# Optimization experiments

Measured on AMD Instinct MI355X. Metric: run time of the kernel, lower is better.

The kernel has to match this reference:

```python
import jax, jax.numpy as jnp
import numpy as np

N = 20000      # nodes
E = 50000      # edges
B = 128        # graphs in batch
H = 64         # hidden_dim
FEAT = 28      # raw node feature dim
N_TYPES = 100  # one-hot size for node_type
EDGE_DIM = 5   # one-hot size for edge_type
OUT = 1        # output_dim
MP_ITER = 3
S2S_ITER = 4


def setup_inputs() -> dict:
    key = jax.random.key(0)
    ks = jax.random.split(key, 24)
    s = 0.05
    inp = {
        'node_feat': jax.random.normal(ks[0], (N, FEAT), dtype=jnp.float32),
        'node_type': jax.random.randint(ks[1], (N,), 0, N_TYPES),
        'edge_index': jax.random.randint(ks[2], (2, E), 0, N),
        'edge_type': jax.random.randint(ks[3], (E,), 0, EDGE_DIM),
        'batch': jnp.sort(jax.random.randint(ks[4], (N,), 0, B)),
        # node embedding
        'W_emb': jax.random.normal(ks[5], (N_TYPES + FEAT, H), dtype=jnp.float32) * s,
        'b_emb': jnp.zeros((H,), dtype=jnp.float32),
        # shared edge net: edge_dim -> H -> H*H
        'W_e1': jax.random.normal(ks[6], (EDGE_DIM, H), dtype=jnp.float32) * s,
        'b_e1': jnp.zeros((H,), dtype=jnp.float32),
        'W_e2': jax.random.normal(ks[7], (H, H * H), dtype=jnp.float32) * s,
        'b_e2': jnp.zeros((H * H,), dtype=jnp.float32),
        # per-layer NNConv root weight + bias
        'roots': jax.random.normal(ks[8], (MP_ITER, H, H), dtype=jnp.float32) * s,
        'conv_bias': jnp.zeros((MP_ITER, H), dtype=jnp.float32),
        # Set2Set LSTM (input 2H, hidden H); torch gate order i,f,g,o
        'W_ih': jax.random.normal(ks[9], (4 * H, 2 * H), dtype=jnp.float32) * s,
        'W_hh': jax.random.normal(ks[10], (4 * H, H), dtype=jnp.float32) * s,
        'b_ih': jnp.zeros((4 * H,), dtype=jnp.float32),
        'b_hh': jnp.zeros((4 * H,), dtype=jnp.float32),
        # output MLP 2H -> H -> OUT
        'W_o1': jax.random.normal(ks[11], (2 * H, H), dtype=jnp.float32) * s,
        'b_o1': jnp.zeros((H,), dtype=jnp.float32),
        'W_o2': jax.random.normal(ks[12], (H, OUT), dtype=jnp.float32) * s,
        'b_o2': jnp.zeros((OUT,), dtype=jnp.float32),
    }
    return inp


def _forward(node_feat, W_emb, b_emb, W_e1, b_e1, W_e2, b_e2, roots, conv_bias,
             W_ih, W_hh, b_ih, b_hh, W_o1, b_o1, W_o2, b_o2,
             node_type, edge_index, edge_type, batch):
    # node embedding: [one_hot(node_type,100) ; node_feat] @ W_emb
    x_in = jnp.concatenate(
        [jax.nn.one_hot(node_type, N_TYPES, dtype=node_feat.dtype), node_feat], axis=-1)
    h = x_in @ W_emb + b_emb                                   # [N, H]

    # edge-conditioned weights (edge_attr is fixed, edge_net is shared across
    # iterations, so nn(edge_attr) is identical each layer -> compute once)
    edge_attr = jax.nn.one_hot(edge_type, EDGE_DIM, dtype=node_feat.dtype)
    Wmat = jax.nn.relu(edge_attr @ W_e1 + b_e1) @ W_e2 + b_e2  # [E, H*H]
    Wmat = Wmat.reshape(E, H, H)                               # [E, H_in, H_out]

    src, dst = edge_index[0], edge_index[1]
    for i in range(MP_ITER):
        msg = jnp.einsum('eh,eho->eo', h[src], Wmat)           # per-edge matvec
        agg = jax.ops.segment_sum(msg, dst, num_segments=N)    # sum aggregation
        h = agg + h @ roots[i] + conv_bias[i]                  # NNConv root + bias

    # Set2Set pooling
    hx = jnp.zeros((B, H), dtype=h.dtype)
    cx = jnp.zeros((B, H), dtype=h.dtype)
    q_star = jnp.zeros((B, 2 * H), dtype=h.dtype)
    for _ in range(S2S_ITER):
        gates = q_star @ W_ih.T + b_ih + hx @ W_hh.T + b_hh
        ig, fg, gg, og = jnp.split(gates, 4, axis=-1)
        cx = jax.nn.sigmoid(fg) * cx + jax.nn.sigmoid(ig) * jnp.tanh(gg)
        hx = jax.nn.sigmoid(og) * jnp.tanh(cx)
        q = hx                                                 # [B, H]
        e = jnp.sum(h * q[batch], axis=-1)                     # [N]
        m = jax.lax.stop_gradient(jax.ops.segment_max(e, batch, num_segments=B))
        a = jnp.exp(e - m[batch])
        denom = jax.ops.segment_sum(a, batch, num_segments=B)
        denom = jnp.where(denom == 0, 1.0, denom)
        a = a / denom[batch]                                   # scatter softmax
        r = jax.ops.segment_sum(a[:, None] * h, batch, num_segments=B)  # [B, H]
        q_star = jnp.concatenate([q, r], axis=-1)

    out = jax.nn.relu(q_star @ W_o1 + b_o1) @ W_o2 + b_o2      # [B, OUT]
    return out


def reference(node_feat, node_type, edge_index, edge_type, batch,
              W_emb, b_emb, W_e1, b_e1, W_e2, b_e2, roots, conv_bias,
              W_ih, W_hh, b_ih, b_hh, W_o1, b_o1, W_o2, b_o2):
    return _forward(node_feat, W_emb, b_emb, W_e1, b_e1, W_e2, b_e2, roots,
                    conv_bias, W_ih, W_hh, b_ih, b_hh, W_o1, b_o1, W_o2, b_o2,
                    node_type, edge_index, edge_type, batch)
```

## Files before the change

### kernel.cpp

```cpp
#include <hip/hip_runtime.h>
#include <math.h>


#define NN 20000
#define NE 50000
#define NB 128
#define HD 64
#define NFEAT 28
#define NTYPES 100
#define EDIM 5
#define MPIT 3
#define S2SIT 4
#define NBLK_E ((NE + 255) / 256)
#define SMAX 224
#define HP (HD + 1)
#define EPW 7

__device__ __forceinline__ float sigm(float x) {
  return 1.0f / (1.0f + expf(-x));
}

__device__ __forceinline__ float rdlane(float v, int l) {
  return __uint_as_float(__builtin_amdgcn_readlane(__float_as_uint(v), l));
}

__global__ __launch_bounds__(256) void k_pre(
    const int* __restrict__ batch, const int* __restrict__ etype,
    int* __restrict__ gstart, int* __restrict__ bc) {
  __shared__ int wcc[4][EDIM];
  const int tid = threadIdx.x;
  const int lane = tid & 63;
  const int wv = tid >> 6;
  const int blk = blockIdx.x;
  const int gtid = (blk << 8) + tid;
  const int nthr = gridDim.x << 8;

  if (blk < NBLK_E) {
    int e = (blk << 8) + tid;
    int ty = (e < NE) ? etype[e] : -1;
    #pragma unroll
    for (int t = 0; t < EDIM; ++t) {
      unsigned long long m = __ballot(ty == t);
      if (lane == 0) wcc[wv][t] = __popcll(m);
    }
    __syncthreads();
    if (tid < EDIM)
      bc[blk * EDIM + tid] = wcc[0][tid] + wcc[1][tid] + wcc[2][tid] + wcc[3][tid];
  }

  for (int n = gtid; n < NN; n += nthr) {
    int b = batch[n];
    if (n == 0)
      for (int t = 0; t <= b; ++t) gstart[t] = 0;
    int bn = (n + 1 < NN) ? batch[n + 1] : NB;
    for (int t = b + 1; t <= bn; ++t) gstart[t] = n + 1;
  }
}

__global__ __launch_bounds__(256) void k_main(
    const float* __restrict__ feat, const int* __restrict__ ntype,
    const int* __restrict__ etype, const int* __restrict__ ei,
    const float* __restrict__ W_emb, const float* __restrict__ b_emb,
    const float* __restrict__ W_e1, const float* __restrict__ b_e1,
    const float* __restrict__ W_e2, const float* __restrict__ b_e2,
    const float* __restrict__ W_ih, const float* __restrict__ W_hh,
    const int* __restrict__ bc,
    float* __restrict__ Wty, float* __restrict__ hA, float* __restrict__ hB,
    float* __restrict__ W_ihT, float* __restrict__ W_hhT,
    int2* __restrict__ sd) {
  __shared__ float sv[EDIM][HD];
  __shared__ float red[4][EDIM][HD];
  __shared__ int s_base[EDIM];
  __shared__ int wc[4][EDIM];
  const int tid = threadIdx.x;
  const int lane = tid & 63;
  const int wv = tid >> 6;
  const int blk = blockIdx.x;
  const int nblk = gridDim.x;
  const int nthr = nblk << 8;
  const int gtid = (blk << 8) + tid;
  const int gw = (blk << 2) + wv;
  const int nwave = nblk << 2;

  if (blk < 64) {
    int mbase = blk * 64;
    for (int idx = tid; idx < EDIM * HD; idx += 256) {
      int t = idx >> 6, j = idx & 63;
      float x = W_e1[t * HD + j] + b_e1[j];
      sv[t][j] = x > 0.f ? x : 0.f;
    }
    __syncthreads();
    int l = tid & 63, jg = tid >> 6;
    float acc[EDIM] = {0.f, 0.f, 0.f, 0.f, 0.f};
    #pragma unroll
    for (int jj = 0; jj < 16; ++jj) {
      int j = jg * 16 + jj;
      float w2 = W_e2[j * 4096 + mbase + l];
      #pragma unroll
      for (int t = 0; t < EDIM; ++t) acc[t] = fmaf(sv[t][j], w2, acc[t]);
    }
    #pragma unroll
    for (int t = 0; t < EDIM; ++t) red[jg][t][l] = acc[t];
    __syncthreads();
    for (int idx = tid; idx < EDIM * HD; idx += 256) {
      int t = idx >> 6, m = idx & 63;
      float s = red[0][t][m] + red[1][t][m] + red[2][t][m] + red[3][t][m];
      Wty[t * 4096 + mbase + m] = s + b_e2[mbase + m];
    }
  }

  if (blk >= 64 && blk < 64 + NBLK_E) {
    int pblk = blk - 64;
    if (wv == 0) {
      int part[EDIM], tot[EDIM];
      #pragma unroll
      for (int t = 0; t < EDIM; ++t) { part[t] = 0; tot[t] = 0; }
      for (int b = lane; b < NBLK_E; b += 64) {
        #pragma unroll
        for (int t = 0; t < EDIM; ++t) {
          int x = bc[b * EDIM + t];
          tot[t] += x;
          if (b < pblk) part[t] += x;
        }
      }
      #pragma unroll
      for (int t = 0; t < EDIM; ++t) {
        #pragma unroll
        for (int off = 32; off; off >>= 1) {
          tot[t]  += __shfl_xor(tot[t],  off, 64);
          part[t] += __shfl_xor(part[t], off, 64);
        }
      }
      if (lane == 0) {
        int run = 0;
        #pragma unroll
        for (int t = 0; t < EDIM; ++t) {
          s_base[t] = run + part[t];
          run += tot[t];
        }
      }
    }
    int e = (pblk << 8) + tid;
    int ty = (e < NE) ? etype[e] : -1;
    int svv = 0, dv = 0;
    if (e < NE) { svv = ei[e]; dv = ei[NE + e]; }
    int rank = 0;
    #pragma unroll
    for (int t = 0; t < EDIM; ++t) {
      unsigned long long m = __ballot(ty == t);
      if (lane == 0) wc[wv][t] = __popcll(m);
      if (ty == t) rank = __popcll(m & ((1ull << lane) - 1ull));
    }
    __syncthreads();
    if (ty >= 0) {
      int base = s_base[ty];
      for (int w = 0; w < wv; ++w) base += wc[w][ty];
      sd[base + rank] = make_int2(svv | (ty << 16), dv);
    }
  }

  for (int o = gtid; o < 2 * HD * 4 * HD; o += nthr)
    W_ihT[o] = W_ih[(o & 255) * 128 + (o >> 8)];
  for (int o = gtid; o < HD * 4 * HD; o += nthr)
    W_hhT[o] = W_hh[(o & 255) * 64 + (o >> 8)];

  {
    float wf[NFEAT];
    #pragma unroll
    for (int f = 0; f < NFEAT; ++f) wf[f] = W_emb[(NTYPES + f) * HD + lane];
    float bb = b_emb[lane];
    for (int n = gw; n < NN; n += nwave) {
      int nu = __builtin_amdgcn_readfirstlane(n);
      int t = __builtin_amdgcn_readfirstlane(ntype[nu]);
      const float* row = feat + nu * NFEAT;
      float acc = bb + W_emb[t * HD + lane];
      #pragma unroll
      for (int f = 0; f < NFEAT; ++f) acc = fmaf(row[f], wf[f], acc);
      hA[nu * HD + lane] = acc;
    }
  }

  {
    float4 z = make_float4(0.f, 0.f, 0.f, 0.f);
    for (int i = gtid; i < NN * HD / 4; i += nthr)
      reinterpret_cast<float4*>(hB)[i] = z;
  }
}

__global__ __launch_bounds__(256) void k_mp(
    const int2* __restrict__ sd,
    const float* __restrict__ Wty, const float* __restrict__ hsrc,
    float* __restrict__ htgt, float* __restrict__ hzero,
    const float* __restrict__ root, const float* __restrict__ bias) {
  const int lane = threadIdx.x & 63;
  const int wv = threadIdx.x >> 6;
  const int blk = blockIdx.x;

  if (blk < 512) {
    float w[HD];
    #pragma unroll
    for (int k = 0; k < HD; ++k) w[k] = root[k * HD + lane];
    float bb = bias[lane];
    int rw = (blk << 2) + wv;
    for (int n = rw; n < NN; n += 2048) {
      int nu = __builtin_amdgcn_readfirstlane(n);
      const float* row = hsrc + nu * HD;
      float a0 = bb, a1 = 0.f, a2 = 0.f, a3 = 0.f;
      #pragma unroll
      for (int k = 0; k < HD; k += 4) {
        a0 = fmaf(row[k + 0], w[k + 0], a0);
        a1 = fmaf(row[k + 1], w[k + 1], a1);
        a2 = fmaf(row[k + 2], w[k + 2], a2);
        a3 = fmaf(row[k + 3], w[k + 3], a3);
      }
      atomicAdd(&htgt[nu * HD + lane], (a0 + a1) + (a2 + a3));
    }
    if (hzero) {
      float4 z = make_float4(0.f, 0.f, 0.f, 0.f);
      for (int i = (blk << 8) + threadIdx.x; i < NN * HD / 4; i += 512 * 256)
        reinterpret_cast<float4*>(hzero)[i] = z;
    }
  } else {
    int wid = ((blk - 512) << 2) + wv;
    int beg = wid * EPW;
    if (beg >= NE) return;
    int len = NE - beg; if (len > EPW) len = EPW;

    int2 ed = sd[beg + (lane < len ? lane : len - 1)];

    float hv[EPW];
    #pragma unroll
    for (int j = 0; j < EPW; ++j) {
      int sx = __builtin_amdgcn_readlane(ed.x, j < EPW ? j : 0);
      hv[j] = hsrc[(sx & 0xFFFF) * HD + lane];
    }

    int curt = -1;
    float w[HD];
    #pragma unroll
    for (int j = 0; j < EPW; ++j) {
      if (j >= len) break;
      int ex = __builtin_amdgcn_readlane(ed.x, j);
      int dj = __builtin_amdgcn_readlane(ed.y, j);
      int ty = ex >> 16;
      if (ty != curt) {
        curt = ty;
        #pragma unroll
        for (int k = 0; k < HD; ++k) w[k] = Wty[ty * 4096 + k * HD + lane];
      }
      float a0 = 0.f, a1 = 0.f, a2 = 0.f, a3 = 0.f;
      #pragma unroll
      for (int k = 0; k < HD; k += 4) {
        a0 = fmaf(rdlane(hv[j], k + 0), w[k + 0], a0);
        a1 = fmaf(rdlane(hv[j], k + 1), w[k + 1], a1);
        a2 = fmaf(rdlane(hv[j], k + 2), w[k + 2], a2);
        a3 = fmaf(rdlane(hv[j], k + 3), w[k + 3], a3);
      }
      atomicAdd(&htgt[dj * HD + lane], (a0 + a1) + (a2 + a3));
    }
  }
}

__global__ __launch_bounds__(256) void k_s2s(
    const float* __restrict__ h, const int* __restrict__ gstart,
    const float* __restrict__ W_ihT, const float* __restrict__ W_hhT,
    const float* __restrict__ b_ih, const float* __restrict__ b_hh,
    const float* __restrict__ W_o1, const float* __restrict__ b_o1,
    const float* __restrict__ W_o2, const float* __restrict__ b_o2,
    float* __restrict__ out) {
  __shared__ float hs[SMAX * HP];
  __shared__ float ebuf[SMAX];
  __shared__ float qstar[2 * HD];
  __shared__ float hxs[HD], cxs[HD], gates[4 * HD];
  __shared__ float redM[4], redS[4], redR[4][HD];
  __shared__ float hid[HD];
  int b = blockIdx.x;
  int tid = threadIdx.x;
  int lane = tid & 63, wv = tid >> 6;

  int st = gstart[b], en = gstart[b + 1];
  int cnt = en - st;
  int cached = cnt < SMAX ? cnt : SMAX;

  int total = cached * HD;
  for (int base = tid * 4; base < total; base += 1024) {
    float4 v = *reinterpret_cast<const float4*>(h + st * HD + base);
    int n = base >> 6, k = base & 63;
    float* row = hs + n * HP + k;
    row[0] = v.x; row[1] = v.y; row[2] = v.z; row[3] = v.w;
  }
  if (tid < 2 * HD) qstar[tid] = 0.f;
  if (tid < HD) { hxs[tid] = 0.f; cxs[tid] = 0.f; }
  __syncthreads();

  for (int it = 0; it < S2SIT; ++it) {
    float acc0 = b_ih[tid] + b_hh[tid], acc1 = 0.f;
    #pragma unroll 8
    for (int j = 0; j < 2 * HD; j += 2) {
      acc0 = fmaf(qstar[j],     W_ihT[j * 256 + tid],       acc0);
      acc1 = fmaf(qstar[j + 1], W_ihT[(j + 1) * 256 + tid], acc1);
    }
    #pragma unroll 8
    for (int j = 0; j < HD; j += 2) {
      acc0 = fmaf(hxs[j],     W_hhT[j * 256 + tid],       acc0);
      acc1 = fmaf(hxs[j + 1], W_hhT[(j + 1) * 256 + tid], acc1);
    }
    gates[tid] = acc0 + acc1;
    __syncthreads();
    if (tid < HD) {
      float ig = sigm(gates[tid]);
      float fg = sigm(gates[HD + tid]);
      float gg = tanhf(gates[2 * HD + tid]);
      float og = sigm(gates[3 * HD + tid]);
      float c = fmaf(fg, cxs[tid], ig * gg);
      cxs[tid] = c;
      hxs[tid] = og * tanhf(c);
    }
    __syncthreads();

    float e = -1e30f;
    if (tid < cached) {
      const float* row = hs + tid * HP;
      float d0 = 0.f, d1 = 0.f;
      #pragma unroll 8
      for (int k = 0; k < HD; k += 2) {
        d0 = fmaf(row[k],     hxs[k],     d0);
        d1 = fmaf(row[k + 1], hxs[k + 1], d1);
      }
      e = d0 + d1;
      ebuf[tid] = e;
    }
    float m = e;
    #pragma unroll
    for (int off = 32; off; off >>= 1) m = fmaxf(m, __shfl_xor(m, off, 64));
    float qreg = hxs[lane];
    for (int n = cached + wv; n < cnt; n += 4) {
      float ev = h[(st + n) * HD + lane] * qreg;
      #pragma unroll
      for (int off = 32; off; off >>= 1) ev += __shfl_xor(ev, off, 64);
      m = fmaxf(m, ev);
    }
    if (lane == 0) redM[wv] = m;
    __syncthreads();
    float M = fmaxf(fmaxf(redM[0], redM[1]), fmaxf(redM[2], redM[3]));

    float sp = 0.f;
    if (tid < cached) {
      float a = expf(ebuf[tid] - M);
      ebuf[tid] = a;
      sp = a;
    }
    #pragma unroll
    for (int off = 32; off; off >>= 1) sp += __shfl_xor(sp, off, 64);
    __syncthreads();

    float r = 0.f;
    for (int n = wv; n < cached; n += 4)
      r = fmaf(ebuf[n], hs[n * HP + lane], r);
    float s_tail = 0.f;
    for (int n = cached + wv; n < cnt; n += 4) {
      float v = h[(st + n) * HD + lane];
      float ev = v * qreg;
      #pragma unroll
      for (int off = 32; off; off >>= 1) ev += __shfl_xor(ev, off, 64);
      float a = expf(ev - M);
      s_tail += a;
      r = fmaf(a, v, r);
    }
    if (lane == 0) redS[wv] = sp + s_tail;
    redR[wv][lane] = r;
    __syncthreads();
    if (tid < HD) {
      float S = redS[0] + redS[1] + redS[2] + redS[3];
      float R = redR[0][tid] + redR[1][tid] + redR[2][tid] + redR[3][tid];
      if (S == 0.f) S = 1.f;
      qstar[tid] = hxs[tid];
      qstar[HD + tid] = R / S;
    }
    __syncthreads();
  }

  if (tid < HD) {
    float acc = b_o1[tid];
    #pragma unroll 8
    for (int i = 0; i < 2 * HD; ++i)
      acc = fmaf(qstar[i], W_o1[i * HD + tid], acc);
    hid[tid] = acc > 0.f ? acc : 0.f;
  }
  __syncthreads();
  if (tid < HD) {
    float p = hid[tid] * W_o2[tid];
    #pragma unroll
    for (int off = 32; off; off >>= 1) p += __shfl_xor(p, off, 64);
    if (tid == 0) out[b] = p + b_o2[0];
  }
}

extern "C" void kernel_launch(void* const* d_in, const int* in_sizes, int n_in,
                              void* d_out, int out_size, void* d_ws, size_t ws_size,
                              hipStream_t stream) {
  const float* node_feat = (const float*)d_in[0];
  const int*   node_type = (const int*)d_in[1];
  const int*   edge_index= (const int*)d_in[2];
  const int*   edge_type = (const int*)d_in[3];
  const int*   batch     = (const int*)d_in[4];
  const float* W_emb     = (const float*)d_in[5];
  const float* b_emb     = (const float*)d_in[6];
  const float* W_e1      = (const float*)d_in[7];
  const float* b_e1      = (const float*)d_in[8];
  const float* W_e2      = (const float*)d_in[9];
  const float* b_e2      = (const float*)d_in[10];
  const float* roots     = (const float*)d_in[11];
  const float* conv_bias = (const float*)d_in[12];
  const float* W_ih      = (const float*)d_in[13];
  const float* W_hh      = (const float*)d_in[14];
  const float* b_ih      = (const float*)d_in[15];
  const float* b_hh      = (const float*)d_in[16];
  const float* W_o1      = (const float*)d_in[17];
  const float* b_o1      = (const float*)d_in[18];
  const float* W_o2      = (const float*)d_in[19];
  const float* b_o2      = (const float*)d_in[20];
  float* out = (float*)d_out;

  float* Wty   = (float*)d_ws;
  float* hA    = Wty + EDIM * 4096;
  float* hB    = hA + NN * HD;
  float* hC    = hB + NN * HD;
  float* W_ihT = hC + NN * HD;
  float* W_hhT = W_ihT + 2 * HD * 4 * HD;
  int2*  sd    = (int2*)(W_hhT + HD * 4 * HD);
  int*   gstart= (int*)(sd + NE);
  int*   bc    = gstart + 136;

  k_pre<<<256, 256, 0, stream>>>(batch, edge_type, gstart, bc);
  k_main<<<512, 256, 0, stream>>>(node_feat, node_type, edge_type, edge_index,
                                  W_emb, b_emb, W_e1, b_e1, W_e2, b_e2,
                                  W_ih, W_hh, bc, Wty, hA, hB, W_ihT, W_hhT, sd);

  k_mp<<<2560, 256, 0, stream>>>(sd, Wty, hA, hB, hC,
                                 roots + 0 * HD * HD, conv_bias + 0 * HD);
  k_mp<<<2560, 256, 0, stream>>>(sd, Wty, hB, hC, hA,
                                 roots + 1 * HD * HD, conv_bias + 1 * HD);
  k_mp<<<2560, 256, 0, stream>>>(sd, Wty, hC, hA, (float*)0,
                                 roots + 2 * HD * HD, conv_bias + 2 * HD);

  k_s2s<<<NB, 256, 0, stream>>>(hA, gstart, W_ihT, W_hhT, b_ih, b_hh,
                                W_o1, b_o1, W_o2, b_o2, out);
}
```

Baseline: 203.7 us.

## Drop k_pre kernel; recompute edge-type counts per block and binary-search graph bounds

Result: slower. 334.8 us (+64.3%).

```diff
diff --git a/kernel.cpp b/kernel.cpp
--- a/kernel.cpp
+++ b/kernel.cpp
@@ -12,6 +12,7 @@
 #define MPIT 3
 #define S2SIT 4
 #define NBLK_E ((NE + 255) / 256)
+#define EPAD (NBLK_E * 256)
 #define SMAX 224
 #define HP (HD + 1)
 #define EPW 7
@@ -22,39 +23,6 @@
 
 __device__ __forceinline__ float rdlane(float v, int l) {
   return __uint_as_float(__builtin_amdgcn_readlane(__float_as_uint(v), l));
-}
-
-__global__ __launch_bounds__(256) void k_pre(
-    const int* __restrict__ batch, const int* __restrict__ etype,
-    int* __restrict__ gstart, int* __restrict__ bc) {
-  __shared__ int wcc[4][EDIM];
-  const int tid = threadIdx.x;
-  const int lane = tid & 63;
-  const int wv = tid >> 6;
-  const int blk = blockIdx.x;
-  const int gtid = (blk << 8) + tid;
-  const int nthr = gridDim.x << 8;
-
-  if (blk < NBLK_E) {
-    int e = (blk << 8) + tid;
-    int ty = (e < NE) ? etype[e] : -1;
-    #pragma unroll
-    for (int t = 0; t < EDIM; ++t) {
-      unsigned long long m = __ballot(ty == t);
-      if (lane == 0) wcc[wv][t] = __popcll(m);
-    }
-    __syncthreads();
-    if (tid < EDIM)
-      bc[blk * EDIM + tid] = wcc[0][tid] + wcc[1][tid] + wcc[2][tid] + wcc[3][tid];
-  }
-
-  for (int n = gtid; n < NN; n += nthr) {
-    int b = batch[n];
-    if (n == 0)
-      for (int t = 0; t <= b; ++t) gstart[t] = 0;
-    int bn = (n + 1 < NN) ? batch[n + 1] : NB;
-    for (int t = b + 1; t <= bn; ++t) gstart[t] = n + 1;
-  }
 }
 
 __global__ __launch_bounds__(256) void k_main(
@@ -64,13 +32,13 @@
     const float* __restrict__ W_e1, const float* __restrict__ b_e1,
     const float* __restrict__ W_e2, const float* __restrict__ b_e2,
     const float* __restrict__ W_ih, const float* __restrict__ W_hh,
-    const int* __restrict__ bc,
     float* __restrict__ Wty, float* __restrict__ hA, float* __restrict__ hB,
     float* __restrict__ W_ihT, float* __restrict__ W_hhT,
     int2* __restrict__ sd) {
   __shared__ float sv[EDIM][HD];
   __shared__ float red[4][EDIM][HD];
   __shared__ int s_base[EDIM];
+  __shared__ int s_part[EDIM], s_tot[EDIM];
   __shared__ int wc[4][EDIM];
   const int tid = threadIdx.x;
   const int lane = tid & 63;
@@ -111,36 +79,33 @@
 
   if (blk >= 64 && blk < 64 + NBLK_E) {
     int pblk = blk - 64;
-    if (wv == 0) {
-      int part[EDIM], tot[EDIM];
-      #pragma unroll
-      for (int t = 0; t < EDIM; ++t) { part[t] = 0; tot[t] = 0; }
-      for (int b = lane; b < NBLK_E; b += 64) {
-        #pragma unroll
-        for (int t = 0; t < EDIM; ++t) {
-          int x = bc[b * EDIM + t];
-          tot[t] += x;
-          if (b < pblk) part[t] += x;
+    int plim = pblk << 8;
+    if (tid < EDIM) { s_part[tid] = 0; s_tot[tid] = 0; }
+    __syncthreads();
+    for (int i = tid; i < EPAD; i += 256) {
+      int ty2 = (i < NE) ? etype[i] : -1;
+      #pragma unroll
+      for (int t = 0; t < EDIM; ++t) {
+        unsigned long long m  = __ballot(ty2 == t);
+        unsigned long long mp = __ballot(ty2 == t && i < plim);
+        if (lane == 0) {
+          if (m)  atomicAdd(&s_tot[t],  __popcll(m));
+          if (mp) atomicAdd(&s_part[t], __popcll(mp));
         }
       }
+    }
+    __syncthreads();
+    if (tid == 0) {
+      int run = 0;
       #pragma unroll
       for (int t = 0; t < EDIM; ++t) {
-        #pragma unroll
-        for (int off = 32; off; off >>= 1) {
-          tot[t]  += __shfl_xor(tot[t],  off, 64);
-          part[t] += __shfl_xor(part[t], off, 64);
-        }
-      }
-      if (lane == 0) {
-        int run = 0;
-        #pragma unroll
-        for (int t = 0; t < EDIM; ++t) {
-          s_base[t] = run + part[t];
-          run += tot[t];
-        }
-      }
-    }
-    int e = (pblk << 8) + tid;
+        s_base[t] = run + s_part[t];
+        run += s_tot[t];
+      }
+    }
+    __syncthreads();
+
+    int e = plim + tid;
     int ty = (e < NE) ? etype[e] : -1;
     int svv = 0, dv = 0;
     if (e < NE) { svv = ei[e]; dv = ei[NE + e]; }
@@ -262,7 +227,7 @@
 }
 
 __global__ __launch_bounds__(256) void k_s2s(
-    const float* __restrict__ h, const int* __restrict__ gstart,
+    const float* __restrict__ h, const int* __restrict__ batch,
     const float* __restrict__ W_ihT, const float* __restrict__ W_hhT,
     const float* __restrict__ b_ih, const float* __restrict__ b_hh,
     const float* __restrict__ W_o1, const float* __restrict__ b_o1,
@@ -274,11 +239,22 @@
   __shared__ float hxs[HD], cxs[HD], gates[4 * HD];
   __shared__ float redM[4], redS[4], redR[4][HD];
   __shared__ float hid[HD];
+  __shared__ int s_st, s_en;
   int b = blockIdx.x;
   int tid = threadIdx.x;
   int lane = tid & 63, wv = tid >> 6;
 
-  int st = gstart[b], en = gstart[b + 1];
+  if (tid < 2) {
+    int key = b + tid;
+    int lo = 0, hi = NN;
+    while (lo < hi) {
+      int mid = (lo + hi) >> 1;
+      if (batch[mid] < key) lo = mid + 1; else hi = mid;
+    }
+    if (tid == 0) s_st = lo; else s_en = lo;
+  }
+  __syncthreads();
+  int st = s_st, en = s_en;
   int cnt = en - st;
   int cached = cnt < SMAX ? cnt : SMAX;
 
@@ -429,13 +405,10 @@
   float* W_ihT = hC + NN * HD;
   float* W_hhT = W_ihT + 2 * HD * 4 * HD;
   int2*  sd    = (int2*)(W_hhT + HD * 4 * HD);
-  int*   gstart= (int*)(sd + NE);
-  int*   bc    = gstart + 136;
-
-  k_pre<<<256, 256, 0, stream>>>(batch, edge_type, gstart, bc);
+
   k_main<<<512, 256, 0, stream>>>(node_feat, node_type, edge_type, edge_index,
                                   W_emb, b_emb, W_e1, b_e1, W_e2, b_e2,
-                                  W_ih, W_hh, bc, Wty, hA, hB, W_ihT, W_hhT, sd);
+                                  W_ih, W_hh, Wty, hA, hB, W_ihT, W_hhT, sd);
 
   k_mp<<<2560, 256, 0, stream>>>(sd, Wty, hA, hB, hC,
                                  roots + 0 * HD * HD, conv_bias + 0 * HD);
@@ -444,6 +417,6 @@
   k_mp<<<2560, 256, 0, stream>>>(sd, Wty, hC, hA, (float*)0,
                                  roots + 2 * HD * HD, conv_bias + 2 * HD);
 
-  k_s2s<<<NB, 256, 0, stream>>>(hA, gstart, W_ihT, W_hhT, b_ih, b_hh,
+  k_s2s<<<NB, 256, 0, stream>>>(hA, batch, W_ihT, W_hhT, b_ih, b_hh,
                                 W_o1, b_o1, W_o2, b_o2, out);
 }
```
